# Performance work log

Hardware: AMD Instinct MI355X
Metric: run time of the kernel (lower is better)

The kernel has to match this reference:

```python
import jax, jax.numpy as jnp
import numpy as np

V, E, H, B, S = 50257, 512, 512, 64, 2048


def setup_inputs() -> dict:
    key = jax.random.key(0)
    ks = jax.random.split(key, 12)
    w = lambda k, shape: jax.random.normal(k, shape, dtype=jnp.float32) * 0.02
    return {
        "input_seq": jax.random.randint(ks[0], (1, B), 0, V),
        "last_hidden": jax.random.normal(ks[1], (1, B, H), dtype=jnp.float32),
        "encoder_outputs": jax.random.normal(ks[2], (S, B, H), dtype=jnp.float32),
        "emb": w(ks[3], (V, E)),
        "w_ih": w(ks[4], (3 * H, E)),
        "w_hh": w(ks[5], (3 * H, H)),
        "b_ih": jnp.zeros((3 * H,), jnp.float32),
        "b_hh": jnp.zeros((3 * H,), jnp.float32),
        "w_concat": w(ks[6], (H, 2 * H)),
        "b_concat": jnp.zeros((H,), jnp.float32),
        "w_out": w(ks[7], (V, H)),
        "b_out": jnp.zeros((V,), jnp.float32),
    }


def gru_step(x, h, w_ih, w_hh, b_ih, b_hh):
    # PyTorch GRU cell: gates ordered [r, z, n]
    gi = x @ w_ih.T + b_ih  # [B, 3H]
    gh = h @ w_hh.T + b_hh  # [B, 3H]
    i_r, i_z, i_n = jnp.split(gi, 3, axis=1)
    h_r, h_z, h_n = jnp.split(gh, 3, axis=1)
    r = jax.nn.sigmoid(i_r + h_r)
    z = jax.nn.sigmoid(i_z + h_z)
    n = jnp.tanh(i_n + r * h_n)
    return (1.0 - z) * n + z * h


def reference(input_seq, last_hidden, encoder_outputs, emb, w_ih, w_hh,
              b_ih, b_hh, w_concat, b_concat, w_out, b_out):
    x = emb[input_seq[0]]            # [B, E] embedding lookup (seq len 1)
    h = last_hidden[0]               # [B, H]
    h_new = gru_step(x, h, w_ih, w_hh, b_ih, b_hh)  # [B, H]
    hidden = h_new[None]             # [1, B, H]
    rnn_output = h_new               # [B, H]
    # 'dot' attention: energies[b, s] = <rnn_output[b], encoder_outputs[s, b]>
    energies = jnp.einsum('bh,sbh->bs', rnn_output, encoder_outputs)
    attn = jax.nn.softmax(energies, axis=1)          # [B, S]
    context = jnp.einsum('bs,sbh->bh', attn, encoder_outputs)  # [B, H]
    concat_output = jnp.tanh(
        jnp.concatenate([rnn_output, context], axis=1) @ w_concat.T + b_concat)
    output = concat_output @ w_out.T + b_out         # [B, V]
    return output, hidden, attn[:, None, :]
```

## Files before the change

kernel.cpp:

```cpp
#include <hip/hip_runtime.h>
#include <math.h>

#define NB 64
#define NS 2048
#define NH 512
#define NE 512
#define NV 50257
#define H3 1536
#define KSL 8
#define NCH 32

typedef __attribute__((ext_vector_type(8))) short bf16x8;
typedef __attribute__((ext_vector_type(4))) float f32x4;

#define GI_OFF    0
#define GH_OFF    (GI_OFF + KSL*H3*NB)
#define HNEW_OFF  (GH_OFF + KSL*H3*NB)
#define EN_OFF    (HNEW_OFF + NB*NH)
#define PCTX_OFF  (EN_OFF + NB*NS)
#define PM_OFF    (PCTX_OFF + NB*NCH*NH)
#define PL_OFF    (PM_OFF + NB*NCH)
#define CPART_OFF (PL_OFF + NB*NCH)
#define CTX_OFF   (CPART_OFF + 4*NH*NB)
#define CCB_OFF   (CTX_OFF + NB*NH)

#define HID_OFF  ((size_t)NB*NV)
#define ATTN_OFF (HID_OFF + (size_t)NB*NH)

__device__ __forceinline__ unsigned short f2bf(float f) {
    unsigned u = __builtin_bit_cast(unsigned, f);
    u += 0x7FFFu + ((u >> 16) & 1u);
    return (unsigned short)(u >> 16);
}

__global__ __launch_bounds__(256) void k1_gru_gemm(
    const int* __restrict__ seq, const float* __restrict__ lh,
    const float* __restrict__ emb, const float* __restrict__ wih,
    const float* __restrict__ whh, float* __restrict__ ws)
{
    __shared__ float xl[64][65];
    __shared__ float hl[64][65];
    __shared__ int idxl[64];
    const int t = threadIdx.x;
    const int b = t & 63;
    const int j0 = __builtin_amdgcn_readfirstlane(blockIdx.x * 16 + (t >> 6) * 4);
    const int k0 = blockIdx.y * 64;
    if (t < 64) idxl[t] = seq[t];
    __syncthreads();
    {
        const int r = t >> 2;
        const int c = (t & 3) * 16;
        #pragma unroll
        for (int q = 0; q < 4; ++q) {
            const float4 xv = *(const float4*)&emb[(size_t)idxl[r] * NE + k0 + c + q*4];
            const float4 hv = *(const float4*)&lh[r * NH + k0 + c + q*4];
            xl[r][c+q*4+0]=xv.x; xl[r][c+q*4+1]=xv.y; xl[r][c+q*4+2]=xv.z; xl[r][c+q*4+3]=xv.w;
            hl[r][c+q*4+0]=hv.x; hl[r][c+q*4+1]=hv.y; hl[r][c+q*4+2]=hv.z; hl[r][c+q*4+3]=hv.w;
        }
    }
    __syncthreads();
    float ai[4] = {0.f,0.f,0.f,0.f};
    float ah[4] = {0.f,0.f,0.f,0.f};
    #pragma unroll 4
    for (int e = 0; e < 64; e += 4) {
        const float x0=xl[b][e], x1=xl[b][e+1], x2=xl[b][e+2], x3=xl[b][e+3];
        const float h0=hl[b][e], h1=hl[b][e+1], h2=hl[b][e+2], h3=hl[b][e+3];
        #pragma unroll
        for (int jj = 0; jj < 4; ++jj) {
            const float4 wi = *(const float4*)&wih[(size_t)(j0+jj)*NE + k0 + e];
            const float4 wh = *(const float4*)&whh[(size_t)(j0+jj)*NH + k0 + e];
            ai[jj] = fmaf(x0,wi.x, fmaf(x1,wi.y, fmaf(x2,wi.z, fmaf(x3,wi.w, ai[jj]))));
            ah[jj] = fmaf(h0,wh.x, fmaf(h1,wh.y, fmaf(h2,wh.z, fmaf(h3,wh.w, ah[jj]))));
        }
    }
    float* gi = ws + GI_OFF + (size_t)blockIdx.y * H3 * NB;
    float* gh = ws + GH_OFF + (size_t)blockIdx.y * H3 * NB;
    #pragma unroll
    for (int jj = 0; jj < 4; ++jj) {
        gi[(j0+jj)*NB + b] = ai[jj];
        gh[(j0+jj)*NB + b] = ah[jj];
    }
}

__global__ __launch_bounds__(256) void k2_gates(
    const float* __restrict__ lh, const float* __restrict__ bih,
    const float* __restrict__ bhh, float* __restrict__ ws, float* __restrict__ out)
{
    const int gid = blockIdx.x * 256 + threadIdx.x;
    const int b = gid & 63;
    const int h = gid >> 6;
    const float* gi = ws + GI_OFF;
    const float* gh = ws + GH_OFF;
    const int P = H3 * NB;
    float ir = bih[h], iz = bih[512+h], inn = bih[1024+h];
    float hr = bhh[h], hz = bhh[512+h], hnn = bhh[1024+h];
    #pragma unroll
    for (int s = 0; s < KSL; ++s) {
        ir  += gi[s*P + h*NB + b];
        iz  += gi[s*P + (512+h)*NB + b];
        inn += gi[s*P + (1024+h)*NB + b];
        hr  += gh[s*P + h*NB + b];
        hz  += gh[s*P + (512+h)*NB + b];
        hnn += gh[s*P + (1024+h)*NB + b];
    }
    const float r = 1.f / (1.f + __expf(-(ir + hr)));
    const float z = 1.f / (1.f + __expf(-(iz + hz)));
    const float nx = inn + r * hnn;
    const float e2 = __expf(-2.f * fabsf(nx));
    const float n = copysignf((1.f - e2) / (1.f + e2), nx);
    const float hnew = (1.f - z) * n + z * lh[b*NH + h];
    ws[HNEW_OFF + b*NH + h] = hnew;
    out[HID_OFF + (size_t)b*NH + h] = hnew;
}

__global__ __launch_bounds__(256) void k3_attn(
    const float* __restrict__ enc, float* __restrict__ ws)
{
    const int t = threadIdx.x;
    const int w = t >> 6;
    const int l = t & 63;
    const int b = blockIdx.x >> 5;
    const int chunk = blockIdx.x & 31;
    const float* hn = ws + HNEW_OFF + b * NH;
    const float4 hq0 = *(const float4*)&hn[l*4];
    const float4 hq1 = *(const float4*)&hn[256 + l*4];
    const int s0 = chunk * 64 + w * 16;
    const float* rowb = enc + ((size_t)s0 * NB + b) * NH;
    float m = -INFINITY, lsum = 0.f;
    float cx[8] = {0.f,0.f,0.f,0.f,0.f,0.f,0.f,0.f};
    float ekeep = 0.f;
    f32x4 a0 = __builtin_nontemporal_load((const f32x4*)&rowb[l*4]);
    f32x4 a1 = __builtin_nontemporal_load((const f32x4*)&rowb[256 + l*4]);
    for (int i = 0; i < 16; ++i) {
        const f32x4 r0 = a0, r1 = a1;
        if (i < 15) {
            const float* nr = rowb + (size_t)(i+1) * NB * NH;
            a0 = __builtin_nontemporal_load((const f32x4*)&nr[l*4]);
            a1 = __builtin_nontemporal_load((const f32x4*)&nr[256 + l*4]);
        }
        float d = r0.x*hq0.x;
        d = fmaf(r0.y,hq0.y,d); d = fmaf(r0.z,hq0.z,d); d = fmaf(r0.w,hq0.w,d);
        d = fmaf(r1.x,hq1.x,d); d = fmaf(r1.y,hq1.y,d); d = fmaf(r1.z,hq1.z,d); d = fmaf(r1.w,hq1.w,d);
        d += __shfl_xor(d, 32);
        d += __shfl_xor(d, 16);
        d += __shfl_xor(d, 8);
        d += __shfl_xor(d, 4);
        d += __shfl_xor(d, 2);
        d += __shfl_xor(d, 1);
        if (l == i) ekeep = d;
        const float mn = fmaxf(m, d);
        if (mn > m) {
            const float sc = __expf(m - mn);
            lsum *= sc;
            #pragma unroll
            for (int k = 0; k < 8; ++k) cx[k] *= sc;
            m = mn;
        }
        const float p = __expf(d - m);
        lsum += p;
        cx[0]=fmaf(p,r0.x,cx[0]); cx[1]=fmaf(p,r0.y,cx[1]);
        cx[2]=fmaf(p,r0.z,cx[2]); cx[3]=fmaf(p,r0.w,cx[3]);
        cx[4]=fmaf(p,r1.x,cx[4]); cx[5]=fmaf(p,r1.y,cx[5]);
        cx[6]=fmaf(p,r1.z,cx[6]); cx[7]=fmaf(p,r1.w,cx[7]);
    }
    if (l < 16) ws[EN_OFF + (size_t)b * NS + s0 + l] = ekeep;
    __shared__ float ctxl[4][NH];
    __shared__ float ml[4], ll[4];
    #pragma unroll
    for (int k = 0; k < 4; ++k) {
        ctxl[w][l*4+k]       = cx[k];
        ctxl[w][256 + l*4+k] = cx[4+k];
    }
    if (l == 0) { ml[w] = m; ll[w] = lsum; }
    __syncthreads();
    const float M = fmaxf(fmaxf(ml[0], ml[1]), fmaxf(ml[2], ml[3]));
    const float w0 = __expf(ml[0]-M), w1 = __expf(ml[1]-M);
    const float w2 = __expf(ml[2]-M), w3 = __expf(ml[3]-M);
    for (int e = t; e < NH; e += 256) {
        const float c = ctxl[0][e]*w0 + ctxl[1][e]*w1 + ctxl[2][e]*w2 + ctxl[3][e]*w3;
        ws[PCTX_OFF + ((size_t)b*NCH + chunk)*NH + e] = c;
    }
    if (t == 0) {
        ws[PM_OFF + b*NCH + chunk] = M;
        ws[PL_OFF + b*NCH + chunk] = ll[0]*w0 + ll[1]*w1 + ll[2]*w2 + ll[3]*w3;
    }
}

__global__ __launch_bounds__(256) void k4_combine(
    float* __restrict__ ws, float* __restrict__ out)
{
    const int b = blockIdx.x;
    const int sl = blockIdx.y;
    const int t = threadIdx.x;
    __shared__ float pml[NCH], pll[NCH], pwl[NCH];
    if (t < NCH) { pml[t] = ws[PM_OFF + b*NCH + t]; pll[t] = ws[PL_OFF + b*NCH + t]; }
    __syncthreads();
    float M = -INFINITY;
    #pragma unroll
    for (int c = 0; c < NCH; ++c) M = fmaxf(M, pml[c]);
    if (t < NCH) pwl[t] = __expf(pml[t] - M);
    __syncthreads();
    float L = 0.f;
    #pragma unroll
    for (int c = 0; c < NCH; ++c) L += pll[c] * pwl[c];
    const float invL = 1.f / L;
    const int e = sl * 128 + (t & 127);
    if (t < 128) {
        float acc = 0.f;
        #pragma unroll 8
        for (int c = 0; c < NCH; ++c)
            acc += ws[PCTX_OFF + ((size_t)b*NCH + c)*NH + e] * pwl[c];
        ws[CTX_OFF + b*NH + e] = acc * invL;
    }
    for (int s = sl * 512 + t; s < sl * 512 + 512; s += 256)
        out[ATTN_OFF + (size_t)b*NS + s] = __expf(ws[EN_OFF + (size_t)b*NS + s] - M) * invL;
}

__global__ __launch_bounds__(256) void k5_concat_gemm(
    const float* __restrict__ wcat, float* __restrict__ ws)
{
    __shared__ float al[64][65];
    const int t = threadIdx.x;
    const int b = t & 63;
    const int j0 = __builtin_amdgcn_readfirstlane(blockIdx.x * 16 + (t >> 6) * 4);
    const int kc = blockIdx.y;
    const float* A = ws + ((kc < 2) ? HNEW_OFF : CTX_OFF);
    const int kb = (kc & 1) * 256;
    float acc[4] = {0.f,0.f,0.f,0.f};
    const int c4 = (t & 15) * 4;
    const int r0 = t >> 4;
    for (int ch = 0; ch < 4; ++ch) {
        const int k0 = kb + ch * 64;
        __syncthreads();
        #pragma unroll
        for (int i = 0; i < 4; ++i) {
            const int r = r0 + i * 16;
            const float4 v = *(const float4*)&A[r * NH + k0 + c4];
            al[r][c4+0]=v.x; al[r][c4+1]=v.y; al[r][c4+2]=v.z; al[r][c4+3]=v.w;
        }
        __syncthreads();
        #pragma unroll 4
        for (int e = 0; e < 64; e += 4) {
            const float a0v=al[b][e], a1v=al[b][e+1], a2v=al[b][e+2], a3v=al[b][e+3];
            #pragma unroll
            for (int jj = 0; jj < 4; ++jj) {
                const float4 wq = *(const float4*)&wcat[(size_t)(j0+jj)*1024 + kc*256 + ch*64 + e];
                acc[jj] = fmaf(a0v,wq.x, fmaf(a1v,wq.y, fmaf(a2v,wq.z, fmaf(a3v,wq.w, acc[jj]))));
            }
        }
    }
    #pragma unroll
    for (int jj = 0; jj < 4; ++jj)
        ws[CPART_OFF + ((size_t)kc*NH + j0+jj)*NB + b] = acc[jj];
}

__global__ __launch_bounds__(256) void k5b_concat_fin(
    const float* __restrict__ bcat, float* __restrict__ ws)
{
    const int t = threadIdx.x;
    const int b = t & 63;
    const int j = blockIdx.x * 4 + (t >> 6);
    float v = bcat[j];
    #pragma unroll
    for (int kc = 0; kc < 4; ++kc)
        v += ws[CPART_OFF + ((size_t)kc*NH + j)*NB + b];
    const float e2 = __expf(-2.f * fabsf(v));
    const float th = copysignf((1.f - e2) / (1.f + e2), v);
    unsigned short* ccb = (unsigned short*)(ws + CCB_OFF);
    ccb[b*NH + j] = f2bf(th);
}

__global__ __launch_bounds__(256) void k6_mfma(
    const float* __restrict__ wout, const float* __restrict__ bout,
    const unsigned short* __restrict__ ccb, float* __restrict__ out)
{
    __shared__ unsigned short al[64 * 256];
    const int t = threadIdx.x;
    const int w = t >> 6;
    const int l = t & 63;
    const int lm = l & 15;
    const int kg = l >> 4;
    const int j = blockIdx.x * 64 + w * 16 + lm;
    const int jc = j < NV ? j : NV - 1;
    const float* wrow = wout + (size_t)jc * NH + kg * 8;
    f32x4 acc0 = {0.f,0.f,0.f,0.f};
    f32x4 acc1 = {0.f,0.f,0.f,0.f};
    f32x4 acc2 = {0.f,0.f,0.f,0.f};
    f32x4 acc3 = {0.f,0.f,0.f,0.f};
    char* alb = (char*)al;
    #pragma unroll
    for (int ph = 0; ph < 2; ++ph) {
        if (ph) __syncthreads();
        #pragma unroll
        for (int i = 0; i < 8; ++i) {
            const int c = i * 256 + t;
            const int row = c >> 5;
            const int cu = (c & 31) * 8;
            const uint4 v = *(const uint4*)&ccb[row * NH + ph * 256 + cu];
            const int dst = (row * 512 + cu * 2) ^ ((row & 7) << 4);
            *(uint4*)(alb + dst) = v;
        }
        __syncthreads();
        #pragma unroll
        for (int k8 = 0; k8 < 8; ++k8) {
            const int ks = ph * 8 + k8;
            const float4 w0 = *(const float4*)(wrow + ks * 32);
            const float4 w1 = *(const float4*)(wrow + ks * 32 + 4);
            bf16x8 bf;
            bf[0] = (short)f2bf(w0.x); bf[1] = (short)f2bf(w0.y);
            bf[2] = (short)f2bf(w0.z); bf[3] = (short)f2bf(w0.w);
            bf[4] = (short)f2bf(w1.x); bf[5] = (short)f2bf(w1.y);
            bf[6] = (short)f2bf(w1.z); bf[7] = (short)f2bf(w1.w);
            const int kb = k8 * 64 + kg * 16;
            const int r0 = lm,      s0 = (r0 * 512 + kb) ^ ((r0 & 7) << 4);
            const int r1 = 16 + lm, s1 = (r1 * 512 + kb) ^ ((r1 & 7) << 4);
            const int r2 = 32 + lm, s2 = (r2 * 512 + kb) ^ ((r2 & 7) << 4);
            const int r3 = 48 + lm, s3 = (r3 * 512 + kb) ^ ((r3 & 7) << 4);
            const bf16x8 a0 = *(const bf16x8*)(alb + s0);
            const bf16x8 a1 = *(const bf16x8*)(alb + s1);
            const bf16x8 a2 = *(const bf16x8*)(alb + s2);
            const bf16x8 a3 = *(const bf16x8*)(alb + s3);
            acc0 = __builtin_amdgcn_mfma_f32_16x16x32_bf16(a0, bf, acc0, 0, 0, 0);
            acc1 = __builtin_amdgcn_mfma_f32_16x16x32_bf16(a1, bf, acc1, 0, 0, 0);
            acc2 = __builtin_amdgcn_mfma_f32_16x16x32_bf16(a2, bf, acc2, 0, 0, 0);
            acc3 = __builtin_amdgcn_mfma_f32_16x16x32_bf16(a3, bf, acc3, 0, 0, 0);
        }
    }
    if (j < NV) {
        const float bj = bout[jc];
        #pragma unroll
        for (int r = 0; r < 4; ++r) {
            out[(size_t)(0*16 + kg*4 + r) * NV + j] = acc0[r] + bj;
            out[(size_t)(1*16 + kg*4 + r) * NV + j] = acc1[r] + bj;
            out[(size_t)(2*16 + kg*4 + r) * NV + j] = acc2[r] + bj;
            out[(size_t)(3*16 + kg*4 + r) * NV + j] = acc3[r] + bj;
        }
    }
}

extern "C" void kernel_launch(void* const* d_in, const int* in_sizes, int n_in,
                              void* d_out, int out_size, void* d_ws, size_t ws_size,
                              hipStream_t stream) {
    (void)in_sizes; (void)n_in; (void)out_size; (void)ws_size;
    const int*   seq  = (const int*)  d_in[0];
    const float* lh   = (const float*)d_in[1];
    const float* enc  = (const float*)d_in[2];
    const float* emb  = (const float*)d_in[3];
    const float* wih  = (const float*)d_in[4];
    const float* whh  = (const float*)d_in[5];
    const float* bih  = (const float*)d_in[6];
    const float* bhh  = (const float*)d_in[7];
    const float* wcat = (const float*)d_in[8];
    const float* bcat = (const float*)d_in[9];
    const float* wout = (const float*)d_in[10];
    const float* bout = (const float*)d_in[11];
    float* out = (float*)d_out;
    float* ws  = (float*)d_ws;

    k1_gru_gemm <<<dim3(96, KSL), 256, 0, stream>>>(seq, lh, emb, wih, whh, ws);
    k2_gates    <<<128, 256, 0, stream>>>(lh, bih, bhh, ws, out);
    k3_attn     <<<2048, 256, 0, stream>>>(enc, ws);
    k4_combine  <<<dim3(64, 4), 256, 0, stream>>>(ws, out);
    k5_concat_gemm<<<dim3(32, 4), 256, 0, stream>>>(wcat, ws);
    k5b_concat_fin<<<128, 256, 0, stream>>>(bcat, ws);
    k6_mfma     <<<786, 256, 0, stream>>>(wout, bout,
                     (const unsigned short*)(ws + CCB_OFF), out);
}
```

Measured before the change: 114.1 us.

## Fuse context combine, concat GEMM and tanh into one kernel per batch row

Merges the softmax combine, the split-K concat GEMM and its finalize kernel into a single kernel with one block per (batch, half of output columns). Each block rebuilds the full context vector in shared memory, then each thread computes one concat output with a dot product over 1024 inputs and applies tanh before writing bf16. This removes two launches and the partial-sum round trip through the workspace, but every block now reads whole wcat rows (each row read by 64 blocks), uses only 128 blocks, and recomputes the context for each half.

```diff
diff --git a/kernel.cpp b/kernel.cpp
--- a/kernel.cpp
+++ b/kernel.cpp
@@ -20,9 +20,7 @@
 #define PCTX_OFF  (EN_OFF + NB*NS)
 #define PM_OFF    (PCTX_OFF + NB*NCH*NH)
 #define PL_OFF    (PM_OFF + NB*NCH)
-#define CPART_OFF (PL_OFF + NB*NCH)
-#define CTX_OFF   (CPART_OFF + 4*NH*NB)
-#define CCB_OFF   (CTX_OFF + NB*NH)
+#define CCB_OFF   (PL_OFF + NB*NCH)
 
 #define HID_OFF  ((size_t)NB*NV)
 #define ATTN_OFF (HID_OFF + (size_t)NB*NH)
@@ -186,86 +184,49 @@
     }
 }
 
-__global__ __launch_bounds__(256) void k4_combine(
+__global__ __launch_bounds__(256) void kD_ctx_concat(
+    const float* __restrict__ wcat, const float* __restrict__ bcat,
     float* __restrict__ ws, float* __restrict__ out)
 {
     const int b = blockIdx.x;
-    const int sl = blockIdx.y;
+    const int jsl = blockIdx.y;
     const int t = threadIdx.x;
-    __shared__ float pml[NCH], pll[NCH], pwl[NCH];
-    if (t < NCH) { pml[t] = ws[PM_OFF + b*NCH + t]; pll[t] = ws[PL_OFF + b*NCH + t]; }
+    __shared__ float pwl[NCH];
+    __shared__ float hx[1024];
+    if (t < NCH) pwl[t] = ws[PM_OFF + b*NCH + t];
     __syncthreads();
     float M = -INFINITY;
     #pragma unroll
-    for (int c = 0; c < NCH; ++c) M = fmaxf(M, pml[c]);
-    if (t < NCH) pwl[t] = __expf(pml[t] - M);
+    for (int c = 0; c < NCH; ++c) M = fmaxf(M, pwl[c]);
+    __syncthreads();
+    if (t < NCH) pwl[t] = __expf(pwl[t] - M);
     __syncthreads();
     float L = 0.f;
     #pragma unroll
-    for (int c = 0; c < NCH; ++c) L += pll[c] * pwl[c];
+    for (int c = 0; c < NCH; ++c) L += ws[PL_OFF + b*NCH + c] * pwl[c];
     const float invL = 1.f / L;
-    const int e = sl * 128 + (t & 127);
-    if (t < 128) {
+    for (int e = t; e < NH; e += 256) {
         float acc = 0.f;
         #pragma unroll 8
         for (int c = 0; c < NCH; ++c)
             acc += ws[PCTX_OFF + ((size_t)b*NCH + c)*NH + e] * pwl[c];
-        ws[CTX_OFF + b*NH + e] = acc * invL;
-    }
-    for (int s = sl * 512 + t; s < sl * 512 + 512; s += 256)
+        hx[512 + e] = acc * invL;
+        hx[e] = ws[HNEW_OFF + b*NH + e];
+    }
+    for (int s = jsl * 1024 + t; s < jsl * 1024 + 1024; s += 256)
         out[ATTN_OFF + (size_t)b*NS + s] = __expf(ws[EN_OFF + (size_t)b*NS + s] - M) * invL;
-}
-
-__global__ __launch_bounds__(256) void k5_concat_gemm(
-    const float* __restrict__ wcat, float* __restrict__ ws)
-{
-    __shared__ float al[64][65];
-    const int t = threadIdx.x;
-    const int b = t & 63;
-    const int j0 = __builtin_amdgcn_readfirstlane(blockIdx.x * 16 + (t >> 6) * 4);
-    const int kc = blockIdx.y;
-    const float* A = ws + ((kc < 2) ? HNEW_OFF : CTX_OFF);
-    const int kb = (kc & 1) * 256;
-    float acc[4] = {0.f,0.f,0.f,0.f};
-    const int c4 = (t & 15) * 4;
-    const int r0 = t >> 4;
-    for (int ch = 0; ch < 4; ++ch) {
-        const int k0 = kb + ch * 64;
-        __syncthreads();
-        #pragma unroll
-        for (int i = 0; i < 4; ++i) {
-            const int r = r0 + i * 16;
-            const float4 v = *(const float4*)&A[r * NH + k0 + c4];
-            al[r][c4+0]=v.x; al[r][c4+1]=v.y; al[r][c4+2]=v.z; al[r][c4+3]=v.w;
-        }
-        __syncthreads();
-        #pragma unroll 4
-        for (int e = 0; e < 64; e += 4) {
-            const float a0v=al[b][e], a1v=al[b][e+1], a2v=al[b][e+2], a3v=al[b][e+3];
-            #pragma unroll
-            for (int jj = 0; jj < 4; ++jj) {
-                const float4 wq = *(const float4*)&wcat[(size_t)(j0+jj)*1024 + kc*256 + ch*64 + e];
-                acc[jj] = fmaf(a0v,wq.x, fmaf(a1v,wq.y, fmaf(a2v,wq.z, fmaf(a3v,wq.w, acc[jj]))));
-            }
-        }
-    }
-    #pragma unroll
-    for (int jj = 0; jj < 4; ++jj)
-        ws[CPART_OFF + ((size_t)kc*NH + j0+jj)*NB + b] = acc[jj];
-}
-
-__global__ __launch_bounds__(256) void k5b_concat_fin(
-    const float* __restrict__ bcat, float* __restrict__ ws)
-{
-    const int t = threadIdx.x;
-    const int b = t & 63;
-    const int j = blockIdx.x * 4 + (t >> 6);
-    float v = bcat[j];
-    #pragma unroll
-    for (int kc = 0; kc < 4; ++kc)
-        v += ws[CPART_OFF + ((size_t)kc*NH + j)*NB + b];
-    const float e2 = __expf(-2.f * fabsf(v));
-    const float th = copysignf((1.f - e2) / (1.f + e2), v);
+    __syncthreads();
+    const int j = jsl * 256 + t;
+    const float4* wr = (const float4*)&wcat[(size_t)j * 1024];
+    float acc = bcat[j];
+    #pragma unroll 8
+    for (int k = 0; k < 256; ++k) {
+        const float4 wv = wr[k];
+        acc = fmaf(hx[k*4+0], wv.x, fmaf(hx[k*4+1], wv.y,
+              fmaf(hx[k*4+2], wv.z, fmaf(hx[k*4+3], wv.w, acc))));
+    }
+    const float e2 = __expf(-2.f * fabsf(acc));
+    const float th = copysignf((1.f - e2) / (1.f + e2), acc);
     unsigned short* ccb = (unsigned short*)(ws + CCB_OFF);
     ccb[b*NH + j] = f2bf(th);
 }
@@ -357,12 +318,10 @@
     float* out = (float*)d_out;
     float* ws  = (float*)d_ws;
 
-    k1_gru_gemm <<<dim3(96, KSL), 256, 0, stream>>>(seq, lh, emb, wih, whh, ws);
-    k2_gates    <<<128, 256, 0, stream>>>(lh, bih, bhh, ws, out);
-    k3_attn     <<<2048, 256, 0, stream>>>(enc, ws);
-    k4_combine  <<<dim3(64, 4), 256, 0, stream>>>(ws, out);
-    k5_concat_gemm<<<dim3(32, 4), 256, 0, stream>>>(wcat, ws);
-    k5b_concat_fin<<<128, 256, 0, stream>>>(bcat, ws);
-    k6_mfma     <<<786, 256, 0, stream>>>(wout, bout,
-                     (const unsigned short*)(ws + CCB_OFF), out);
-}
+    k1_gru_gemm  <<<dim3(96, KSL), 256, 0, stream>>>(seq, lh, emb, wih, whh, ws);
+    k2_gates     <<<128, 256, 0, stream>>>(lh, bih, bhh, ws, out);
+    k3_attn      <<<2048, 256, 0, stream>>>(enc, ws);
+    kD_ctx_concat<<<dim3(64, 2), 256, 0, stream>>>(wcat, bcat, ws, out);
+    k6_mfma      <<<786, 256, 0, stream>>>(wout, bout,
+                      (const unsigned short*)(ws + CCB_OFF), out);
+}
```

New measurement: 125.5 us. 1.1x slower.
